# Kernel tuning notes

Hardware: AMD Instinct MI355X
Metric: run time of the kernel (lower is better)

Reference implementation:

```python
import jax, jax.numpy as jnp
import numpy as np
from jax import lax

T, Nn, K, IN, H1, H2, G, P, HEADS = 64, 2048, 32, 256, 128, 128, 256, 60, 3


def setup_inputs() -> dict:
    key = jax.random.key(0)
    ks = jax.random.split(key, 20)
    s = 0.05  # weight scale to keep activations sane
    return {
        'h': jax.random.normal(ks[0], (T, Nn, IN), jnp.float32),
        'neigh': jax.random.randint(ks[1], (Nn, K), 0, Nn),
        'Npop': jnp.ones((1,), jnp.float32) * 1e6,
        'I': jax.random.uniform(ks[2], (T,), jnp.float32) * 1e4,
        'R': jax.random.uniform(ks[3], (T,), jnp.float32) * 1e4,
        'S': jax.random.uniform(ks[4], (T,), jnp.float32) * 9e5,
        'It': jax.random.uniform(ks[5], (T,), jnp.float32),
        'Rt': jax.random.uniform(ks[6], (T,), jnp.float32),
        'fc1': jax.random.normal(ks[7], (HEADS, IN, H1), jnp.float32) * s,
        'fc2': jax.random.normal(ks[8], (HEADS * H1, H2), jnp.float32) * s,
        'gru_Wih': jax.random.normal(ks[9], (3 * G, H2), jnp.float32) * s,
        'gru_Whh': jax.random.normal(ks[10], (3 * G, G), jnp.float32) * s,
        'gru_bih': jax.random.normal(ks[11], (3 * G,), jnp.float32) * s,
        'gru_bhh': jax.random.normal(ks[12], (3 * G,), jnp.float32) * s,
        'res1_W': jax.random.normal(ks[13], (2 * P, G + 2), jnp.float32) * s,
        'res1_b': jax.random.normal(ks[14], (2 * P,), jnp.float32) * s,
        'res2_W': jax.random.normal(ks[15], (2, G + 2), jnp.float32) * s,
        'res2_b': jax.random.normal(ks[16], (2,), jnp.float32) * s,
        'hx0': jax.random.normal(ks[17], (G,), jnp.float32),
    }


def _input_attention(iz, neigh):
    # cosine^4 edge scores, unnormalized weighted sum of neighbor feats
    src = iz[neigh]                                  # [N,K,d]
    dot = jnp.einsum('nkd,nd->nk', src, iz)
    nsrc = jnp.sqrt(jnp.einsum('nkd,nkd->nk', src, src))
    ndst = jnp.sqrt(jnp.sum(iz * iz, axis=-1))[:, None]
    e = (dot / nsrc / ndst) ** 4                     # [N,K]
    return jnp.einsum('nk,nkd->nd', e, src)


def _gat_head(x, W, neigh):
    # dot-product edge attention + per-node softmax + weighted reduce
    z = x @ W                                        # [N,H]
    src = z[neigh]                                   # [N,K,H]
    e = jnp.einsum('nkd,nd->nk', src, z)             # [N,K]
    a = jax.nn.softmax(e, axis=1)
    return jnp.einsum('nk,nkd->nd', a, src)


def _gru_cell(x, hx, Wih, Whh, bih, bhh):
    gi = Wih @ x + bih                               # [3G]
    gh = Whh @ hx + bhh
    ir, iz, inn = jnp.split(gi, 3)
    hr, hz, hn = jnp.split(gh, 3)
    r = jax.nn.sigmoid(ir + hr)
    zg = jax.nn.sigmoid(iz + hz)
    n = jnp.tanh(inn + r * hn)
    return (1.0 - zg) * n + zg * hx


def reference(h, neigh, Npop, I, R, S, It, Rt, fc1, fc2, gru_Wih, gru_Whh,
              gru_bih, gru_bhh, res1_W, res1_b, res2_W, res2_b, hx0):
    Np = Npop[0]

    def step(hx, xs):
        h_t, I_t, R_t, S_t, It_t, Rt_t = xs
        ih = _input_attention(h_t, neigh)                       # [N,in]
        heads = jax.vmap(lambda W: _gat_head(ih, W, neigh))(fc1)  # [3,N,H1]
        c = jax.nn.relu(jnp.transpose(heads, (1, 0, 2)).reshape(Nn, HEADS * H1))
        c = _gat_head(c, fc2, neigh)                            # [N,H2]
        pooled = jnp.max(jax.nn.relu(c), axis=0)                # [H2]
        hx = _gru_cell(pooled, hx, gru_Wih, gru_Whh, gru_bih, gru_bhh)
        nhx = jnp.concatenate([hx, It_t[None], Rt_t[None]])     # [G+2]
        pred = res1_W @ nhx + res1_b                            # [2P]
        ab = res2_W @ nhx + res2_b
        a_s = jax.nn.sigmoid(ab[0])
        b_s = jax.nn.sigmoid(ab[1])
        new_I = pred[0::2]
        new_R = pred[1::2]

        def sir(st, _):
            lI, lR, lS = st
            dI = a_s * lI * (lS / Np) - b_s * lI
            dR = b_s * lI
            nI = lI + lax.stop_gradient(dI)
            nR = lR + lax.stop_gradient(dR)
            nS = Np - nI - nR
            return (nI, nR, nS), (dI, dR)

        _, (pI, pR) = lax.scan(sir, (I_t, R_t, S_t), None, length=P)
        return hx, (new_I, new_R, pI, pR)

    _, (new_I, new_R, phy_I, phy_R) = lax.scan(step, hx0, (h, I, R, S, It, Rt))
    return (new_I, new_R, phy_I.reshape(-1), phy_R.reshape(-1))
```

## Files before the change

### kernel.cpp

```cpp
#include <hip/hip_runtime.h>
#include <hip/hip_bf16.h>
#include <math.h>

#define T_STEPS 64
#define NN      2048
#define KN      32
#define IND     256
#define H1D     128
#define C1D     384
#define H2D     128
#define GD      256
#define PD      60
#define GRU_NB  8

#define BITREV5_INIT {0,16,8,24,4,20,12,28,2,18,10,26,6,22,14,30, \
                      1,17,9,25,5,21,13,29,3,19,11,27,7,23,15,31}

__device__ __forceinline__ float bcast_lane(float v, int lane_imm) {
    return __uint_as_float(__builtin_amdgcn_readlane(__float_as_uint(v), lane_imm));
}

__device__ __forceinline__ float xpose_reduce16(float part[16], int lane) {
#pragma unroll
    for (int i = 0; i < 8; ++i) {
        float send = (lane & 2) ? part[i] : part[i + 8];
        float keep = (lane & 2) ? part[i + 8] : part[i];
        part[i] = keep + __shfl_xor(send, 2);
    }
#pragma unroll
    for (int i = 0; i < 4; ++i) {
        float send = (lane & 4) ? part[i] : part[i + 4];
        float keep = (lane & 4) ? part[i + 4] : part[i];
        part[i] = keep + __shfl_xor(send, 4);
    }
#pragma unroll
    for (int i = 0; i < 2; ++i) {
        float send = (lane & 8) ? part[i] : part[i + 2];
        float keep = (lane & 8) ? part[i + 2] : part[i];
        part[i] = keep + __shfl_xor(send, 8);
    }
    {
        float send = (lane & 16) ? part[0] : part[1];
        float keep = (lane & 16) ? part[1] : part[0];
        part[0] = keep + __shfl_xor(send, 16);
    }
    return part[0] + __shfl_xor(part[0], 32);
}

__global__ __launch_bounds__(256) void norms_kernel(const float* __restrict__ h,
                                                    float* __restrict__ norms,
                                                    int t_base) {
    int gw   = (int)((blockIdx.x * blockDim.x + threadIdx.x) >> 6);
    int lane = threadIdx.x & 63;
    int n    = gw & (NN - 1);
    int tloc = gw >> 11;
    const float* row = h + ((size_t)(t_base + tloc) * NN + n) * IND;
    float s = 0.f;
#pragma unroll
    for (int q = 0; q < 4; ++q) { float v = row[lane + 64 * q]; s += v * v; }
#pragma unroll
    for (int off = 32; off > 0; off >>= 1) s += __shfl_xor(s, off);
    if (lane == 0) norms[(size_t)tloc * NN + n] = sqrtf(s);
}

__global__ __launch_bounds__(256, 4) void input_attn_kernel(const float* __restrict__ h,
                                                            const int* __restrict__ neigh,
                                                            const float* __restrict__ norms,
                                                            float* __restrict__ ih,
                                                            int t_base) {
    const int BR[32] = BITREV5_INIT;
    __shared__ float hd_s[2][2][32];
    int wave    = threadIdx.x >> 6;
    int nodeloc = wave >> 1;
    int half    = wave & 1;
    int lane    = threadIdx.x & 63;
    int gw   = (int)((blockIdx.x << 1) | nodeloc);
    int n    = gw & (NN - 1);
    int tloc = gw >> 11;
    const float* hT  = h + (size_t)(t_base + tloc) * NN * IND;
    const float* nrm = norms + (size_t)tloc * NN;

    const float* dst = hT + (size_t)n * IND + half * 128;
    float d0 = dst[lane], d1 = dst[lane + 64];

    int   jreg = neigh[n * KN + (lane & 31)];
    float nj   = nrm[jreg];
    float ndst = nrm[n];

    float r0[32], r1[32], comb[16];
#pragma unroll
    for (int i = 0; i < 16; ++i) {
        int sja = __builtin_amdgcn_readlane(jreg, BR[i]);
        int sjb = __builtin_amdgcn_readlane(jreg, BR[i + 16]);
        const float* sa = hT + (size_t)sja * IND + half * 128;
        const float* sb = hT + (size_t)sjb * IND + half * 128;
        r0[i]      = sa[lane]; r1[i]      = sa[lane + 64];
        r0[i + 16] = sb[lane]; r1[i + 16] = sb[lane + 64];
        float pa = r0[i] * d0 + r1[i] * d1;
        float pb = r0[i + 16] * d0 + r1[i + 16] * d1;
        float send = (lane & 1) ? pa : pb;
        float keep = (lane & 1) ? pb : pa;
        comb[i] = keep + __shfl_xor(send, 1);
    }
#pragma unroll
    for (int i = 0; i < 32; ++i) asm volatile("" : "+v"(r0[i]), "+v"(r1[i]));
    float hdot = xpose_reduce16(comb, lane);
    if (lane < 32) hd_s[nodeloc][half][lane] = hdot;
    __syncthreads();
    float dot = hdot + hd_s[nodeloc][half ^ 1][lane & 31];

    float r  = dot / (nj * ndst);
    float r2 = r * r;
    float e  = r2 * r2;

    float a0 = 0.f, a1 = 0.f;
#pragma unroll
    for (int i = 0; i < 32; ++i) {
        float ek = bcast_lane(e, BR[i]);
        a0 += ek * r0[i];
        a1 += ek * r1[i];
    }
    float* orow = ih + (size_t)gw * IND + half * 128;
    orow[lane]      = a0;
    orow[lane + 64] = a1;
}

__global__ __launch_bounds__(256) void matmul_f32(const float* __restrict__ A,
                                                  const float* __restrict__ B,
                                                  float* __restrict__ C,
                                                  int M, int N, int K) {
    __shared__ float As[16][65];
    __shared__ float Bs[16][68];
    int tid  = threadIdx.x;
    int row0 = blockIdx.y * 64;
    int col0 = blockIdx.x * 64;
    int tr = tid >> 4, tc = tid & 15;
    float acc[4][4] = {};
    int la_m = tid >> 2;
    int la_k = (tid & 3) * 4;
    int lb_k = tid >> 4;
    int lb_n = (tid & 15) * 4;
    for (int k0 = 0; k0 < K; k0 += 16) {
        float4 av = *(const float4*)(A + (size_t)(row0 + la_m) * K + k0 + la_k);
        float4 bv = *(const float4*)(B + (size_t)(k0 + lb_k) * N + col0 + lb_n);
        __syncthreads();
        As[la_k + 0][la_m] = av.x; As[la_k + 1][la_m] = av.y;
        As[la_k + 2][la_m] = av.z; As[la_k + 3][la_m] = av.w;
        *(float4*)&Bs[lb_k][lb_n] = bv;
        __syncthreads();
#pragma unroll
        for (int kk = 0; kk < 16; ++kk) {
            float a[4], b[4];
#pragma unroll
            for (int r = 0; r < 4; ++r) a[r] = As[kk][tr * 4 + r];
#pragma unroll
            for (int c = 0; c < 4; ++c) b[c] = Bs[kk][tc * 4 + c];
#pragma unroll
            for (int r = 0; r < 4; ++r)
#pragma unroll
                for (int c = 0; c < 4; ++c) acc[r][c] += a[r] * b[c];
        }
    }
#pragma unroll
    for (int r = 0; r < 4; ++r) {
        float4 v = { acc[r][0], acc[r][1], acc[r][2], acc[r][3] };
        *(float4*)(C + (size_t)(row0 + tr * 4 + r) * N + col0 + tc * 4) = v;
    }
}

__global__ __launch_bounds__(192, 4) void gat_heads_kernel(const float* __restrict__ z1,
                                                           const int* __restrict__ neigh,
                                                           float* __restrict__ c) {
    const int BR[32] = BITREV5_INIT;
    int n    = blockIdx.x & (NN - 1);
    const float* ztbl = z1 + (size_t)(blockIdx.x >> 11) * NN * C1D;
    int head = threadIdx.x >> 6;
    int lane = threadIdx.x & 63;

    const float* dst = ztbl + (size_t)n * C1D + head * H1D;
    float d0 = dst[lane], d1 = dst[lane + 64];
    int jreg = neigh[n * KN + (lane & 31)];

    float r0[32], r1[32], comb[16];
#pragma unroll
    for (int i = 0; i < 16; ++i) {
        int sja = __builtin_amdgcn_readlane(jreg, BR[i]);
        int sjb = __builtin_amdgcn_readlane(jreg, BR[i + 16]);
        const float* sa = ztbl + (size_t)sja * C1D + head * H1D;
        const float* sb = ztbl + (size_t)sjb * C1D + head * H1D;
        r0[i]      = sa[lane]; r1[i]      = sa[lane + 64];
        r0[i + 16] = sb[lane]; r1[i + 16] = sb[lane + 64];
        float pa = r0[i] * d0 + r1[i] * d1;
        float pb = r0[i + 16] * d0 + r1[i + 16] * d1;
        float send = (lane & 1) ? pa : pb;
        float keep = (lane & 1) ? pb : pa;
        comb[i] = keep + __shfl_xor(send, 1);
    }
#pragma unroll
    for (int i = 0; i < 32; ++i) asm volatile("" : "+v"(r0[i]), "+v"(r1[i]));
    float dot = xpose_reduce16(comb, lane);

    float m = dot;
#pragma unroll
    for (int off = 16; off > 0; off >>= 1) m = fmaxf(m, __shfl_xor(m, off));
    float p = __expf(dot - m);
    float s = p;
#pragma unroll
    for (int off = 16; off > 0; off >>= 1) s += __shfl_xor(s, off);
    p /= s;

    float a0 = 0.f, a1 = 0.f;
#pragma unroll
    for (int i = 0; i < 32; ++i) {
        float pk = bcast_lane(p, BR[i]);
        a0 += pk * r0[i];
        a1 += pk * r1[i];
    }
    size_t base = (size_t)blockIdx.x * C1D + (size_t)head * H1D;
    c[base + lane]      = fmaxf(a0, 0.f);
    c[base + lane + 64] = fmaxf(a1, 0.f);
}

__global__ __launch_bounds__(256, 4) void gat_final_kernel(const float* __restrict__ z2,
                                                           const int* __restrict__ neigh,
                                                           float* __restrict__ c2) {
    const int BR[32] = BITREV5_INIT;
    int gw   = (int)((blockIdx.x << 2) | (threadIdx.x >> 6));
    int n    = gw & (NN - 1);
    const float* ztbl = z2 + (size_t)(gw >> 11) * NN * H2D;
    int lane = threadIdx.x & 63;

    const float* dst = ztbl + (size_t)n * H2D;
    float d0 = dst[lane], d1 = dst[lane + 64];
    int jreg = neigh[n * KN + (lane & 31)];

    float r0[32], r1[32], comb[16];
#pragma unroll
    for (int i = 0; i < 16; ++i) {
        int sja = __builtin_amdgcn_readlane(jreg, BR[i]);
        int sjb = __builtin_amdgcn_readlane(jreg, BR[i + 16]);
        const float* sa = ztbl + (size_t)sja * H2D;
        const float* sb = ztbl + (size_t)sjb * H2D;
        r0[i]      = sa[lane]; r1[i]      = sa[lane + 64];
        r0[i + 16] = sb[lane]; r1[i + 16] = sb[lane + 64];
        float pa = r0[i] * d0 + r1[i] * d1;
        float pb = r0[i + 16] * d0 + r1[i + 16] * d1;
        float send = (lane & 1) ? pa : pb;
        float keep = (lane & 1) ? pb : pa;
        comb[i] = keep + __shfl_xor(send, 1);
    }
#pragma unroll
    for (int i = 0; i < 32; ++i) asm volatile("" : "+v"(r0[i]), "+v"(r1[i]));
    float dot = xpose_reduce16(comb, lane);

    float m = dot;
#pragma unroll
    for (int off = 16; off > 0; off >>= 1) m = fmaxf(m, __shfl_xor(m, off));
    float p = __expf(dot - m);
    float s = p;
#pragma unroll
    for (int off = 16; off > 0; off >>= 1) s += __shfl_xor(s, off);
    p /= s;

    float a0 = 0.f, a1 = 0.f;
#pragma unroll
    for (int i = 0; i < 32; ++i) {
        float pk = bcast_lane(p, BR[i]);
        a0 += pk * r0[i];
        a1 += pk * r1[i];
    }
    c2[(size_t)gw * H2D + lane]      = fmaxf(a0, 0.f);
    c2[(size_t)gw * H2D + lane + 64] = fmaxf(a1, 0.f);
}

__global__ __launch_bounds__(128) void pool_part_kernel(const float* __restrict__ c2,
                                                        float* __restrict__ ppart) {
    int j = threadIdx.x;
    int tloc  = blockIdx.x >> 4;
    int slice = blockIdx.x & 15;
    const float* base = c2 + ((size_t)tloc * NN + slice * 128) * H2D;
    float mx = 0.f;
    for (int q = 0; q < 128; ++q) mx = fmaxf(mx, base[(size_t)q * H2D + j]);
    ppart[(size_t)blockIdx.x * H2D + j] = mx;
}
__global__ __launch_bounds__(128) void pool_reduce_kernel(const float* __restrict__ ppart,
                                                          float* __restrict__ pooled,
                                                          int t_base) {
    int j = threadIdx.x;
    const float* base = ppart + (size_t)blockIdx.x * 16 * H2D;
    float mx = 0.f;
#pragma unroll
    for (int q = 0; q < 16; ++q) mx = fmaxf(mx, base[(size_t)q * H2D + j]);
    pooled[(t_base + blockIdx.x) * H2D + j] = mx;
}

__global__ void prep_W1(const float* __restrict__ fc1, float* __restrict__ W1,
                        unsigned int* __restrict__ cnt) {
    int i = blockIdx.x * 256 + threadIdx.x;
    if (i < 256 * 384) {
        int d = i / 384, cf = i % 384;
        int hd = cf >> 7, j = cf & 127;
        W1[i] = fc1[(size_t)hd * 256 * 128 + (size_t)d * 128 + j];
    }
    if (i < T_STEPS) cnt[i] = 0u;
}

__global__ __launch_bounds__(256) void gi_all_kernel(const float* __restrict__ Wih,
                                                     const float* __restrict__ bih,
                                                     const float* __restrict__ pooled,
                                                     float* __restrict__ gi_all) {
    __shared__ float p_s[H2D];
    int t  = blockIdx.x / 3;
    int ob = (blockIdx.x % 3) * 256;
    if (threadIdx.x < H2D) p_s[threadIdx.x] = pooled[t * H2D + threadIdx.x];
    __syncthreads();
    int o = ob + threadIdx.x;
    float acc = bih[o];
    const float* wr = Wih + (size_t)o * H2D;
#pragma unroll 4
    for (int d = 0; d < H2D; ++d) acc += wr[d] * p_s[d];
    gi_all[t * 768 + o] = acc;
}

__global__ __launch_bounds__(768) void gru_reg_kernel(const float* __restrict__ Whh,
                                                      const float* __restrict__ bhh,
                                                      const float* __restrict__ gi_all,
                                                      const float* __restrict__ hx0,
                                                      float* hx_all,
                                                      unsigned int* cnt) {
    __shared__ float4 hx_pad[72];
    __shared__ __align__(16) float hx_lin[GD];
    __shared__ float gh_s[96];
    int b   = blockIdx.x;
    int tid = threadIdx.x;
    int row_local = tid >> 3;
    int sub       = tid & 7;
    int chunk     = row_local >> 5;
    int r_in      = row_local & 31;
    int grow      = chunk * GD + b * 32 + r_in;

    float4 wreg[8];
    const float4* wrow = (const float4*)(Whh + (size_t)grow * GD + sub * 32);
#pragma unroll
    for (int i = 0; i < 8; ++i) wreg[i] = wrow[i];
    float bias = (sub == 0) ? bhh[grow] : 0.f;

    for (int t = 0; t < T_STEPS; ++t) {
        if (t > 0) {
            if (tid == 0) {
                while (__hip_atomic_load(&cnt[t - 1], __ATOMIC_ACQUIRE,
                                         __HIP_MEMORY_SCOPE_AGENT) < GRU_NB)
                    __builtin_amdgcn_s_sleep(1);
            }
            __syncthreads();
        }
        const float* hsrc = (t == 0) ? hx0 : (hx_all + (size_t)(t - 1) * GD);
        if (tid < 64) {
            float4 v;
            v.x = __hip_atomic_load(hsrc + tid * 4 + 0, __ATOMIC_RELAXED, __HIP_MEMORY_SCOPE_AGENT);
            v.y = __hip_atomic_load(hsrc + tid * 4 + 1, __ATOMIC_RELAXED, __HIP_MEMORY_SCOPE_AGENT);
            v.z = __hip_atomic_load(hsrc + tid * 4 + 2, __ATOMIC_RELAXED, __HIP_MEMORY_SCOPE_AGENT);
            v.w = __hip_atomic_load(hsrc + tid * 4 + 3, __ATOMIC_RELAXED, __HIP_MEMORY_SCOPE_AGENT);
            hx_pad[(tid >> 3) * 9 + (tid & 7)] = v;
            ((float4*)hx_lin)[tid] = v;
        }
        __syncthreads();

        float acc = 0.f;
#pragma unroll
        for (int i = 0; i < 8; ++i) {
            float4 hv = hx_pad[sub * 9 + i];
            float4 wv = wreg[i];
            acc += wv.x * hv.x + wv.y * hv.y + wv.z * hv.z + wv.w * hv.w;
        }
        acc += __shfl_xor(acc, 1);
        acc += __shfl_xor(acc, 2);
        acc += __shfl_xor(acc, 4);
        if (sub == 0) gh_s[row_local] = acc + bias;
        __syncthreads();

        if (tid < 32) {
            int u = b * 32 + tid;
            float gi_r = gi_all[t * 768 + u];
            float gi_z = gi_all[t * 768 + 256 + u];
            float gi_n = gi_all[t * 768 + 512 + u];
            float r  = 1.f / (1.f + expf(-(gi_r + gh_s[tid])));
            float zg = 1.f / (1.f + expf(-(gi_z + gh_s[32 + tid])));
            float nn = tanhf(gi_n + r * gh_s[64 + tid]);
            float hnew = (1.f - zg) * nn + zg * hx_lin[u];
            __hip_atomic_store(&hx_all[(size_t)t * GD + u], hnew,
                               __ATOMIC_RELAXED, __HIP_MEMORY_SCOPE_AGENT);
            __threadfence();
        }
        __syncthreads();
        if (tid == 0)
            __hip_atomic_fetch_add(&cnt[t], 1u, __ATOMIC_RELEASE,
                                   __HIP_MEMORY_SCOPE_AGENT);
    }
}

__global__ __launch_bounds__(128) void res_sir_kernel(const float* __restrict__ hx_all,
                                                      const float* __restrict__ It,
                                                      const float* __restrict__ Rt,
                                                      const float* __restrict__ r1W,
                                                      const float* __restrict__ r1b,
                                                      const float* __restrict__ r2W,
                                                      const float* __restrict__ r2b,
                                                      const float* __restrict__ I,
                                                      const float* __restrict__ R,
                                                      const float* __restrict__ S,
                                                      const float* __restrict__ Npop,
                                                      float* __restrict__ out) {
    __shared__ float nhx[258];
    __shared__ float ab_s[2];
    int t = blockIdx.x, tid = threadIdx.x;
    for (int i = tid; i < GD; i += 128) nhx[i] = hx_all[t * GD + i];
    if (tid == 0) { nhx[256] = It[t]; nhx[257] = Rt[t]; }
    __syncthreads();
    if (tid < 120) {
        float acc = r1b[tid];
        const float* wr = r1W + tid * 258;
        for (int d = 0; d < 258; ++d) acc += wr[d] * nhx[d];
        int idx = t * 60 + (tid >> 1);
        if (tid & 1) out[3840 + idx] = acc;
        else         out[idx] = acc;
    }
    if (tid == 120 || tid == 121) {
        int q = tid - 120;
        float acc = r2b[q];
        const float* wr = r2W + q * 258;
        for (int d = 0; d < 258; ++d) acc += wr[d] * nhx[d];
        ab_s[q] = acc;
    }
    __syncthreads();
    if (tid == 0) {
        float a_s = 1.f / (1.f + expf(-ab_s[0]));
        float b_s = 1.f / (1.f + expf(-ab_s[1]));
        float Np = Npop[0];
        float lI = I[t], lR = R[t], lS = S[t];
        for (int p = 0; p < PD; ++p) {
            float dI = a_s * lI * (lS / Np) - b_s * lI;
            float dR = b_s * lI;
            lI += dI;
            lR += dR;
            lS = Np - lI - lR;
            out[7680  + t * 60 + p] = dI;
            out[11520 + t * 60 + p] = dR;
        }
    }
}

extern "C" void kernel_launch(void* const* d_in, const int* in_sizes, int n_in,
                              void* d_out, int out_size, void* d_ws, size_t ws_size,
                              hipStream_t stream) {
    const float* h    = (const float*)d_in[0];
    const int*   ng   = (const int*)  d_in[1];
    const float* Npop = (const float*)d_in[2];
    const float* I_   = (const float*)d_in[3];
    const float* R_   = (const float*)d_in[4];
    const float* S_   = (const float*)d_in[5];
    const float* It   = (const float*)d_in[6];
    const float* Rt   = (const float*)d_in[7];
    const float* fc1  = (const float*)d_in[8];
    const float* fc2  = (const float*)d_in[9];
    const float* gWih = (const float*)d_in[10];
    const float* gWhh = (const float*)d_in[11];
    const float* gbih = (const float*)d_in[12];
    const float* gbhh = (const float*)d_in[13];
    const float* r1W  = (const float*)d_in[14];
    const float* r1b  = (const float*)d_in[15];
    const float* r2W  = (const float*)d_in[16];
    const float* r2b  = (const float*)d_in[17];
    const float* hx0  = (const float*)d_in[18];
    float* out = (float*)d_out;

    char* w = (char*)d_ws;
    float* pooled = (float*)w; w += (size_t)T_STEPS * H2D * 4;
    float* hx_all = (float*)w; w += (size_t)T_STEPS * GD * 4;
    float* W1     = (float*)w; w += (size_t)256 * 384 * 4;
    float* gi_all = (float*)w; w += (size_t)T_STEPS * 768 * 4;
    float* ppart  = (float*)w; w += (size_t)T_STEPS * 16 * H2D * 4;
    unsigned int* cnt = (unsigned int*)w; w += 256;
    size_t fixed = (size_t)(w - (char*)d_ws);

    int Tc = 16;
    while (Tc > 1) {
        size_t need = fixed + (size_t)Tc * (8192 + 2ull * 2048 * 384 * 4);
        if (need <= ws_size) break;
        Tc >>= 1;
    }
    float* norms = (float*)w; w += (size_t)Tc * NN * 4;
    float* bufA  = (float*)w; w += (size_t)Tc * NN * C1D * 4;
    float* bufB  = (float*)w;

    prep_W1<<<(256 * 384 + 255) / 256, 256, 0, stream>>>(fc1, W1, cnt);

    for (int t0 = 0; t0 < T_STEPS; t0 += Tc) {
        int M = Tc * NN;
        norms_kernel      <<<Tc * NN / 4, 256, 0, stream>>>(h, norms, t0);
        input_attn_kernel <<<Tc * NN / 2, 256, 0, stream>>>(h, ng, norms, bufA, t0);
        matmul_f32<<<dim3(384 / 64, M / 64), 256, 0, stream>>>(bufA, W1, bufB, M, 384, 256);
        gat_heads_kernel  <<<Tc * NN, 192, 0, stream>>>(bufB, ng, bufA);
        matmul_f32<<<dim3(128 / 64, M / 64), 256, 0, stream>>>(bufA, fc2, bufB, M, 128, 384);
        gat_final_kernel  <<<Tc * NN / 4, 256, 0, stream>>>(bufB, ng, bufA);
        pool_part_kernel  <<<Tc * 16, 128, 0, stream>>>(bufA, ppart);
        pool_reduce_kernel<<<Tc, 128, 0, stream>>>(ppart, pooled, t0);
    }

    gi_all_kernel<<<T_STEPS * 3, 256, 0, stream>>>(gWih, gbih, pooled, gi_all);
    gru_reg_kernel<<<GRU_NB, 768, 0, stream>>>(gWhh, gbhh, gi_all, hx0, hx_all, cnt);
    res_sir_kernel<<<T_STEPS, 128, 0, stream>>>(hx_all, It, Rt, r1W, r1b, r2W, r2b,
                                                I_, R_, S_, Npop, out);
}
```

Measured before the change: 1.602 ms.

## Interleave timesteps in block indexing, halve chunk size, spread GRU blocks across XCDs

Block indices in the graph kernels now put the timestep in the low bits, so neighbouring blocks handle the same node at different timesteps. This likely targets cache locality or XCD distribution on the chiplet GPU. The time chunk shrinks from 16 to 8, which shrinks the working set but doubles the number of launches. The norms kernel now reads with float4 loads. The GRU launches 8x more blocks and all but every eighth exit immediately, which likely places the live blocks on separate XCDs. A __threadfence after each atomic store is removed, which relies on the later release atomic for ordering.

```diff
diff --git a/kernel.cpp b/kernel.cpp
--- a/kernel.cpp
+++ b/kernel.cpp
@@ -49,15 +49,14 @@
 
 __global__ __launch_bounds__(256) void norms_kernel(const float* __restrict__ h,
                                                     float* __restrict__ norms,
-                                                    int t_base) {
-    int gw   = (int)((blockIdx.x * blockDim.x + threadIdx.x) >> 6);
+                                                    int t_base, int tmask, int tshift) {
+    int b    = blockIdx.x;
+    int tloc = b & tmask;
+    int n    = ((b >> tshift) << 2) | (threadIdx.x >> 6);
     int lane = threadIdx.x & 63;
-    int n    = gw & (NN - 1);
-    int tloc = gw >> 11;
-    const float* row = h + ((size_t)(t_base + tloc) * NN + n) * IND;
-    float s = 0.f;
-#pragma unroll
-    for (int q = 0; q < 4; ++q) { float v = row[lane + 64 * q]; s += v * v; }
+    const float4* row = (const float4*)(h + ((size_t)(t_base + tloc) * NN + n) * IND);
+    float4 v = row[lane];
+    float s = v.x * v.x + v.y * v.y + v.z * v.z + v.w * v.w;
 #pragma unroll
     for (int off = 32; off > 0; off >>= 1) s += __shfl_xor(s, off);
     if (lane == 0) norms[(size_t)tloc * NN + n] = sqrtf(s);
@@ -67,16 +66,16 @@
                                                             const int* __restrict__ neigh,
                                                             const float* __restrict__ norms,
                                                             float* __restrict__ ih,
-                                                            int t_base) {
+                                                            int t_base, int tmask, int tshift) {
     const int BR[32] = BITREV5_INIT;
     __shared__ float hd_s[2][2][32];
     int wave    = threadIdx.x >> 6;
     int nodeloc = wave >> 1;
     int half    = wave & 1;
     int lane    = threadIdx.x & 63;
-    int gw   = (int)((blockIdx.x << 1) | nodeloc);
-    int n    = gw & (NN - 1);
-    int tloc = gw >> 11;
+    int b    = blockIdx.x;
+    int tloc = b & tmask;
+    int n    = (int)(((b >> tshift) << 1) | nodeloc);
     const float* hT  = h + (size_t)(t_base + tloc) * NN * IND;
     const float* nrm = norms + (size_t)tloc * NN;
 
@@ -120,7 +119,7 @@
         a0 += ek * r0[i];
         a1 += ek * r1[i];
     }
-    float* orow = ih + (size_t)gw * IND + half * 128;
+    float* orow = ih + ((size_t)tloc * NN + n) * IND + half * 128;
     orow[lane]      = a0;
     orow[lane + 64] = a1;
 }
@@ -170,10 +169,13 @@
 
 __global__ __launch_bounds__(192, 4) void gat_heads_kernel(const float* __restrict__ z1,
                                                            const int* __restrict__ neigh,
-                                                           float* __restrict__ c) {
+                                                           float* __restrict__ c,
+                                                           int tmask, int tshift) {
     const int BR[32] = BITREV5_INIT;
-    int n    = blockIdx.x & (NN - 1);
-    const float* ztbl = z1 + (size_t)(blockIdx.x >> 11) * NN * C1D;
+    int b    = blockIdx.x;
+    int tloc = b & tmask;
+    int n    = b >> tshift;
+    const float* ztbl = z1 + (size_t)tloc * NN * C1D;
     int head = threadIdx.x >> 6;
     int lane = threadIdx.x & 63;
 
@@ -216,18 +218,20 @@
         a0 += pk * r0[i];
         a1 += pk * r1[i];
     }
-    size_t base = (size_t)blockIdx.x * C1D + (size_t)head * H1D;
+    size_t base = ((size_t)tloc * NN + n) * C1D + (size_t)head * H1D;
     c[base + lane]      = fmaxf(a0, 0.f);
     c[base + lane + 64] = fmaxf(a1, 0.f);
 }
 
 __global__ __launch_bounds__(256, 4) void gat_final_kernel(const float* __restrict__ z2,
                                                            const int* __restrict__ neigh,
-                                                           float* __restrict__ c2) {
+                                                           float* __restrict__ c2,
+                                                           int tmask, int tshift) {
     const int BR[32] = BITREV5_INIT;
-    int gw   = (int)((blockIdx.x << 2) | (threadIdx.x >> 6));
-    int n    = gw & (NN - 1);
-    const float* ztbl = z2 + (size_t)(gw >> 11) * NN * H2D;
+    int b    = blockIdx.x;
+    int tloc = b & tmask;
+    int n    = (int)(((b >> tshift) << 2) | (threadIdx.x >> 6));
+    const float* ztbl = z2 + (size_t)tloc * NN * H2D;
     int lane = threadIdx.x & 63;
 
     const float* dst = ztbl + (size_t)n * H2D;
@@ -269,29 +273,33 @@
         a0 += pk * r0[i];
         a1 += pk * r1[i];
     }
-    c2[(size_t)gw * H2D + lane]      = fmaxf(a0, 0.f);
-    c2[(size_t)gw * H2D + lane + 64] = fmaxf(a1, 0.f);
+    size_t row = (size_t)tloc * NN + n;
+    c2[row * H2D + lane]      = fmaxf(a0, 0.f);
+    c2[row * H2D + lane + 64] = fmaxf(a1, 0.f);
 }
 
 __global__ __launch_bounds__(128) void pool_part_kernel(const float* __restrict__ c2,
-                                                        float* __restrict__ ppart) {
+                                                        float* __restrict__ ppart,
+                                                        int tmask, int tshift) {
     int j = threadIdx.x;
-    int tloc  = blockIdx.x >> 4;
-    int slice = blockIdx.x & 15;
+    int b = blockIdx.x;
+    int tloc  = b & tmask;
+    int slice = b >> tshift;
     const float* base = c2 + ((size_t)tloc * NN + slice * 128) * H2D;
     float mx = 0.f;
     for (int q = 0; q < 128; ++q) mx = fmaxf(mx, base[(size_t)q * H2D + j]);
-    ppart[(size_t)blockIdx.x * H2D + j] = mx;
+    ppart[(size_t)b * H2D + j] = mx;
 }
 __global__ __launch_bounds__(128) void pool_reduce_kernel(const float* __restrict__ ppart,
                                                           float* __restrict__ pooled,
-                                                          int t_base) {
+                                                          int t_base, int tshift) {
     int j = threadIdx.x;
-    const float* base = ppart + (size_t)blockIdx.x * 16 * H2D;
+    int tloc = blockIdx.x;
     float mx = 0.f;
 #pragma unroll
-    for (int q = 0; q < 16; ++q) mx = fmaxf(mx, base[(size_t)q * H2D + j]);
-    pooled[(t_base + blockIdx.x) * H2D + j] = mx;
+    for (int q = 0; q < 16; ++q)
+        mx = fmaxf(mx, ppart[(size_t)((q << tshift) | tloc) * H2D + j]);
+    pooled[(t_base + tloc) * H2D + j] = mx;
 }
 
 __global__ void prep_W1(const float* __restrict__ fc1, float* __restrict__ W1,
@@ -328,10 +336,11 @@
                                                       const float* __restrict__ hx0,
                                                       float* hx_all,
                                                       unsigned int* cnt) {
+    if (blockIdx.x & 7) return;
+    int b = blockIdx.x >> 3;
     __shared__ float4 hx_pad[72];
     __shared__ __align__(16) float hx_lin[GD];
     __shared__ float gh_s[96];
-    int b   = blockIdx.x;
     int tid = threadIdx.x;
     int row_local = tid >> 3;
     int sub       = tid & 7;
@@ -390,7 +399,6 @@
             float hnew = (1.f - zg) * nn + zg * hx_lin[u];
             __hip_atomic_store(&hx_all[(size_t)t * GD + u], hnew,
                                __ATOMIC_RELAXED, __HIP_MEMORY_SCOPE_AGENT);
-            __threadfence();
         }
         __syncthreads();
         if (tid == 0)
@@ -483,12 +491,15 @@
     unsigned int* cnt = (unsigned int*)w; w += 256;
     size_t fixed = (size_t)(w - (char*)d_ws);
 
-    int Tc = 16;
+    int Tc = 8;
     while (Tc > 1) {
         size_t need = fixed + (size_t)Tc * (8192 + 2ull * 2048 * 384 * 4);
         if (need <= ws_size) break;
         Tc >>= 1;
     }
+    int tmask = Tc - 1;
+    int tshift = 0;
+    while ((1 << tshift) < Tc) ++tshift;
     float* norms = (float*)w; w += (size_t)Tc * NN * 4;
     float* bufA  = (float*)w; w += (size_t)Tc * NN * C1D * 4;
     float* bufB  = (float*)w;
@@ -497,18 +508,18 @@
 
     for (int t0 = 0; t0 < T_STEPS; t0 += Tc) {
         int M = Tc * NN;
-        norms_kernel      <<<Tc * NN / 4, 256, 0, stream>>>(h, norms, t0);
-        input_attn_kernel <<<Tc * NN / 2, 256, 0, stream>>>(h, ng, norms, bufA, t0);
+        norms_kernel      <<<Tc * NN / 4, 256, 0, stream>>>(h, norms, t0, tmask, tshift);
+        input_attn_kernel <<<Tc * NN / 2, 256, 0, stream>>>(h, ng, norms, bufA, t0, tmask, tshift);
         matmul_f32<<<dim3(384 / 64, M / 64), 256, 0, stream>>>(bufA, W1, bufB, M, 384, 256);
-        gat_heads_kernel  <<<Tc * NN, 192, 0, stream>>>(bufB, ng, bufA);
+        gat_heads_kernel  <<<Tc * NN, 192, 0, stream>>>(bufB, ng, bufA, tmask, tshift);
         matmul_f32<<<dim3(128 / 64, M / 64), 256, 0, stream>>>(bufA, fc2, bufB, M, 128, 384);
-        gat_final_kernel  <<<Tc * NN / 4, 256, 0, stream>>>(bufB, ng, bufA);
-        pool_part_kernel  <<<Tc * 16, 128, 0, stream>>>(bufA, ppart);
-        pool_reduce_kernel<<<Tc, 128, 0, stream>>>(ppart, pooled, t0);
+        gat_final_kernel  <<<Tc * NN / 4, 256, 0, stream>>>(bufB, ng, bufA, tmask, tshift);
+        pool_part_kernel  <<<Tc * 16, 128, 0, stream>>>(bufA, ppart, tmask, tshift);
+        pool_reduce_kernel<<<Tc, 128, 0, stream>>>(ppart, pooled, t0, tshift);
     }
 
     gi_all_kernel<<<T_STEPS * 3, 256, 0, stream>>>(gWih, gbih, pooled, gi_all);
-    gru_reg_kernel<<<GRU_NB, 768, 0, stream>>>(gWhh, gbhh, gi_all, hx0, hx_all, cnt);
+    gru_reg_kernel<<<GRU_NB * 8, 768, 0, stream>>>(gWhh, gbhh, gi_all, hx0, hx_all, cnt);
     res_sir_kernel<<<T_STEPS, 128, 0, stream>>>(hx_all, It, Rt, r1W, r1b, r2W, r2b,
                                                 I_, R_, S_, Npop, out);
 }
```

After: 1.728 ms. 7.9% more time.
